# Optimization experiments

Measured on AMD Instinct MI355X. Metric: run time of the kernel, lower is better.

Reference implementation:

```python
import jax, jax.numpy as jnp
import numpy as np

EPS = 1e-5
NUM_GROUPS = 32
NUM_HEADS = 8

def group_norm(x, w, b):
    # x: (B, C, H, W), 32 groups, affine per-channel
    B, C, H, W = x.shape
    xg = x.reshape(B, NUM_GROUPS, C // NUM_GROUPS, H, W)
    mu = xg.mean(axis=(2, 3, 4), keepdims=True)
    var = xg.var(axis=(2, 3, 4), keepdims=True)
    xn = ((xg - mu) * jax.lax.rsqrt(var + EPS)).reshape(B, C, H, W)
    return xn * w[None, :, None, None] + b[None, :, None, None]

def conv1x1(x, w, b):
    # 1x1 conv == per-pixel linear; w: (out, in), x: (B, C, H, W)
    return jnp.einsum('oc,bchw->bohw', w, x) + b[None, :, None, None]

def setup_inputs() -> dict:
    key = jax.random.key(0)
    ks = jax.random.split(key, 4)
    B, C, H, W = 2, 512, 64, 64
    s = 1.0 / np.sqrt(C)
    return {
        'x': jax.random.normal(ks[0], (B, C, H, W), jnp.float32),
        'gn_w': jnp.ones((C,), jnp.float32),
        'gn_b': jnp.zeros((C,), jnp.float32),
        'wq': jax.random.normal(ks[1], (C, C), jnp.float32) * s,
        'bq': jnp.zeros((C,), jnp.float32),
        'wkv': jax.random.normal(ks[2], (2 * C, C), jnp.float32) * s,
        'bkv': jnp.zeros((2 * C,), jnp.float32),
        'wo': jax.random.normal(ks[3], (C, C), jnp.float32) * s,
        'bo': jnp.zeros((C,), jnp.float32),
    }

def reference(x, gn_w, gn_b, wq, bq, wkv, bkv, wo, bo):
    B, C, H, W = x.shape
    hd = C // NUM_HEADS  # head_dim
    residual = x
    x_norm = group_norm(x, gn_w, gn_b)
    q = conv1x1(x_norm, wq, bq).reshape(B, NUM_HEADS, hd, H * W)
    kv = conv1x1(x_norm, wkv, bkv)
    k, v = jnp.split(kv, 2, axis=1)
    k = k.reshape(B, NUM_HEADS, hd, H * W)
    v = v.reshape(B, NUM_HEADS, hd, H * W)
    scale = hd ** (-0.5)
    attn = jnp.einsum('bhdi,bhdj->bhij', q, k) * scale
    attn = jax.nn.softmax(attn, axis=-1)
    out = jnp.einsum('bhij,bhdj->bhdi', attn, v).reshape(B, C, H, W)
    out = conv1x1(out, wo, bo)
    return out + residual
```

## Files before the change

kernel.cpp:

```cpp
#include <hip/hip_runtime.h>
#include <cmath>

typedef __bf16 bf16x8 __attribute__((ext_vector_type(8)));
typedef __bf16 bf16x4 __attribute__((ext_vector_type(4)));
typedef float  f32x4  __attribute__((ext_vector_type(4)));

static __device__ __forceinline__ f32x4 mfma16(bf16x8 a, bf16x8 b, f32x4 c) {
    return __builtin_amdgcn_mfma_f32_16x16x32_bf16(a, b, c, 0, 0, 0);
}

static __device__ __forceinline__ float fast_exp2(float x) {
#if __has_builtin(__builtin_amdgcn_exp2f)
    return __builtin_amdgcn_exp2f(x);
#else
    return exp2f(x);
#endif
}

static __device__ __forceinline__ bf16x8 cvt8(float4 a, float4 b) {
    bf16x8 r;
    r[0] = (__bf16)a.x; r[1] = (__bf16)a.y; r[2] = (__bf16)a.z; r[3] = (__bf16)a.w;
    r[4] = (__bf16)b.x; r[5] = (__bf16)b.y; r[6] = (__bf16)b.z; r[7] = (__bf16)b.w;
    return r;
}

#define OFF_STATS 0
#define OFF_XNT   (4096 + 2u*1024*1024)
#define OFF_QKT   (OFF_XNT + 8u*1024*1024)
#define OFF_V     (OFF_QKT + 16u*1024*1024)
#define OFF_OP    (OFF_V + 8u*1024*1024)
#define CHUNK_O   4194304u
#define CHUNK_L   65536u

__global__ __launch_bounds__(256) void gn_stats(const float* __restrict__ x,
                                                float* __restrict__ stats) {
    int blk = blockIdx.x;
    int bg = blk >> 2, chunk = blk & 3;
    const float* base = x + (size_t)bg * 65536 + (size_t)chunk * 16384;
    float s = 0.f, ss = 0.f;
    for (int i = threadIdx.x; i < 4096; i += 256) {
        float4 v = ((const float4*)base)[i];
        s  += v.x + v.y + v.z + v.w;
        ss += v.x*v.x + v.y*v.y + v.z*v.z + v.w*v.w;
    }
    #pragma unroll
    for (int off = 1; off < 64; off <<= 1) {
        s  += __shfl_xor(s,  off);
        ss += __shfl_xor(ss, off);
    }
    __shared__ float red[8];
    int wave = threadIdx.x >> 6;
    if ((threadIdx.x & 63) == 0) { red[wave*2] = s; red[wave*2+1] = ss; }
    __syncthreads();
    if (threadIdx.x == 0) {
        float S  = red[0] + red[2] + red[4] + red[6];
        float SS = red[1] + red[3] + red[5] + red[7];
        atomicAdd(&stats[bg*2],     S);
        atomicAdd(&stats[bg*2 + 1], SS);
    }
}

__global__ __launch_bounds__(256) void gn_apply(const float* __restrict__ x,
                                                const float* __restrict__ stats,
                                                const float* __restrict__ w,
                                                const float* __restrict__ bgn,
                                                __bf16* __restrict__ xnT) {
    int p0 = blockIdx.x * 64, c0 = blockIdx.y * 64, b = blockIdx.z;
    int tid = threadIdx.x, lane = tid & 63, wave = tid >> 6;
    __shared__ float t[64][69];
    #pragma unroll
    for (int i = 0; i < 16; ++i) {
        int cc = i * 4 + wave;
        int c  = c0 + cc;
        int g  = (b << 5) + (c >> 4);
        float mu  = stats[g*2] * (1.f/65536.f);
        float var = stats[g*2+1] * (1.f/65536.f) - mu*mu;
        float rstd = rsqrtf(var + 1e-5f);
        float val = x[((size_t)(b*512 + c) << 12) + p0 + lane];
        t[cc][lane] = (val - mu) * rstd * w[c] + bgn[c];
    }
    __syncthreads();
    #pragma unroll
    for (int i = 0; i < 16; ++i) {
        int pp = i * 4 + wave;
        xnT[((size_t)(b*4096 + p0 + pp) << 9) + c0 + lane] = (__bf16)t[lane][pp];
    }
}

__global__ __launch_bounds__(256) void gemm_qk_kernel(
    const __bf16* __restrict__ A, const float* __restrict__ Wq,
    const float* __restrict__ Wk,
    const float* __restrict__ bq, const float* __restrict__ bk,
    float qscale, __bf16* __restrict__ out) {
    const int bz = blockIdx.z;
    A += (size_t)bz * 2097152;
    const int m0 = blockIdx.x * 128, n0 = blockIdx.y * 128;
    const int tid = threadIdx.x, lane = tid & 63, wave = tid >> 6;
    const int quad = lane >> 4, l16 = lane & 15;
    const int wm = (wave >> 1) * 64, wn = (wave & 1) * 64;
    const int K = 512;

    __shared__ __attribute__((aligned(16))) __bf16 lds_a[128][40];
    __shared__ __attribute__((aligned(16))) __bf16 lds_b[128][40];

    f32x4 acc[4][4];
    #pragma unroll
    for (int mt = 0; mt < 4; ++mt)
        #pragma unroll
        for (int nt = 0; nt < 4; ++nt)
            #pragma unroll
            for (int r = 0; r < 4; ++r) acc[mt][nt][r] = 0.f;

    const int row_s = tid >> 2;
    const int kc    = (tid & 3) << 3;

    const __bf16* Abase = A + (size_t)(m0 + row_s) * K + kc;
    const int br0 = n0 + row_s, br1 = br0 + 64;
    const float* B0 = (br0 < 512) ? (Wq + (size_t)br0 * K + kc) : (Wk + (size_t)(br0 - 512) * K + kc);
    const float* B1 = (br1 < 512) ? (Wq + (size_t)br1 * K + kc) : (Wk + (size_t)(br1 - 512) * K + kc);

    uint4 ra0, ra1;
    float4 f0a, f0b, f1a, f1b;
    ra0 = *(const uint4*)Abase;
    ra1 = *(const uint4*)(Abase + (size_t)64 * K);
    f0a = *(const float4*)B0;      f0b = *(const float4*)(B0 + 4);
    f1a = *(const float4*)B1;      f1b = *(const float4*)(B1 + 4);

    for (int kt = 0; kt < K; kt += 32) {
        *(uint4*)&lds_a[row_s][kc]       = ra0;
        *(uint4*)&lds_a[row_s + 64][kc]  = ra1;
        *(bf16x8*)&lds_b[row_s][kc]      = cvt8(f0a, f0b);
        *(bf16x8*)&lds_b[row_s + 64][kc] = cvt8(f1a, f1b);
        __syncthreads();
        if (kt + 32 < K) {
            ra0 = *(const uint4*)(Abase + kt + 32);
            ra1 = *(const uint4*)(Abase + kt + 32 + (size_t)64 * K);
            f0a = *(const float4*)(B0 + kt + 32); f0b = *(const float4*)(B0 + kt + 36);
            f1a = *(const float4*)(B1 + kt + 32); f1b = *(const float4*)(B1 + kt + 36);
        }
        bf16x8 af[4], bfr[4];
        #pragma unroll
        for (int mt = 0; mt < 4; ++mt)
            af[mt] = *(const bf16x8*)&lds_a[wm + mt*16 + l16][quad*8];
        #pragma unroll
        for (int nt = 0; nt < 4; ++nt)
            bfr[nt] = *(const bf16x8*)&lds_b[wn + nt*16 + l16][quad*8];
        #pragma unroll
        for (int mt = 0; mt < 4; ++mt)
            #pragma unroll
            for (int nt = 0; nt < 4; ++nt)
                acc[mt][nt] = mfma16(af[mt], bfr[nt], acc[mt][nt]);
        __syncthreads();
    }

    #pragma unroll
    for (int mt = 0; mt < 4; ++mt) {
        const int mrow = m0 + wm + mt*16 + quad*4;
        #pragma unroll
        for (int nt = 0; nt < 4; ++nt) {
            const int ncol = n0 + wn + nt*16 + l16;
            #pragma unroll
            for (int r = 0; r < 4; ++r) {
                const int m = mrow + r;
                float bval = (ncol < 512) ? bq[ncol] : bk[ncol - 512];
                float val = acc[mt][nt][r] + bval;
                if (ncol < 512) val *= qscale;
                out[(size_t)bz * 4194304 + (size_t)m * 1024 + ncol] = (__bf16)val;
            }
        }
    }
}

template<int OUT_F32, int HAS_RES>
__global__ __launch_bounds__(256) void gemm64_kernel(
    const float* __restrict__ A, const __bf16* __restrict__ B,
    const float* __restrict__ bias, const float* __restrict__ res,
    void* __restrict__ out,
    int N, int K, long long strideB, long long strideO) {
    const int bz = blockIdx.z;
    B += strideB * bz;
    const int m0 = blockIdx.x * 64, n0 = blockIdx.y * 128;
    const int tid = threadIdx.x, lane = tid & 63, wave = tid >> 6;
    const int quad = lane >> 4, l16 = lane & 15;
    const int wn = wave * 32;

    __shared__ __attribute__((aligned(16))) __bf16 lds_a[64][40];
    __shared__ __attribute__((aligned(16))) __bf16 lds_b[128][40];

    f32x4 acc[4][2];
    #pragma unroll
    for (int mt = 0; mt < 4; ++mt)
        #pragma unroll
        for (int nt = 0; nt < 2; ++nt)
            #pragma unroll
            for (int r = 0; r < 4; ++r) acc[mt][nt][r] = 0.f;

    const int row_s = tid >> 2;
    const int kc    = (tid & 3) << 3;

    const float*  Abase = A + (size_t)(m0 + row_s) * K + kc;
    const __bf16* Bbase = B + (size_t)(n0 + row_s) * K + kc;
    float4 fa, fb;
    uint4 rb0, rb1;
    fa  = *(const float4*)Abase;  fb = *(const float4*)(Abase + 4);
    rb0 = *(const uint4*)Bbase;
    rb1 = *(const uint4*)(Bbase + (size_t)64 * K);

    for (int kt = 0; kt < K; kt += 32) {
        *(bf16x8*)&lds_a[row_s][kc]     = cvt8(fa, fb);
        *(uint4*)&lds_b[row_s][kc]      = rb0;
        *(uint4*)&lds_b[row_s + 64][kc] = rb1;
        __syncthreads();
        if (kt + 32 < K) {
            fa  = *(const float4*)(Abase + kt + 32); fb = *(const float4*)(Abase + kt + 36);
            rb0 = *(const uint4*)(Bbase + kt + 32);
            rb1 = *(const uint4*)(Bbase + kt + 32 + (size_t)64 * K);
        }
        bf16x8 af[4], bfr[2];
        #pragma unroll
        for (int mt = 0; mt < 4; ++mt)
            af[mt] = *(const bf16x8*)&lds_a[mt*16 + l16][quad*8];
        #pragma unroll
        for (int nt = 0; nt < 2; ++nt)
            bfr[nt] = *(const bf16x8*)&lds_b[wn + nt*16 + l16][quad*8];
        #pragma unroll
        for (int mt = 0; mt < 4; ++mt)
            #pragma unroll
            for (int nt = 0; nt < 2; ++nt)
                acc[mt][nt] = mfma16(af[mt], bfr[nt], acc[mt][nt]);
        __syncthreads();
    }

    #pragma unroll
    for (int mt = 0; mt < 4; ++mt) {
        const int mrow = m0 + mt*16 + quad*4;
        #pragma unroll
        for (int nt = 0; nt < 2; ++nt) {
            const int ncol = n0 + wn + nt*16 + l16;
            #pragma unroll
            for (int r = 0; r < 4; ++r) {
                const int m = mrow + r;
                float val = acc[mt][nt][r] + bias[m];
                const size_t idx = (size_t)strideO * bz + (size_t)m * N + ncol;
                if constexpr (HAS_RES) val += res[idx];
                if constexpr (OUT_F32) ((float*)out)[idx] = val;
                else ((__bf16*)out)[idx] = (__bf16)val;
            }
        }
    }
}

template<int NCH>
__global__ __launch_bounds__(256, 3) void attn_kernel(const __bf16* __restrict__ qkT,
                                                      const __bf16* __restrict__ v,
                                                      __bf16* __restrict__ attnT,
                                                      __bf16* __restrict__ Opart,
                                                      float* __restrict__ Lpart) {
    const int b = blockIdx.y >> 3, h = blockIdx.y & 7;
    const int chunk = (NCH > 1) ? blockIdx.z : 0;
    const int NITER = 64 / NCH;
    const int kt0 = chunk * (4096 / NCH);
    const int tid = threadIdx.x;
    const int wave = tid >> 6, lane = tid & 63;
    const int quad = lane >> 4, l16 = lane & 15;
    const int qbase = blockIdx.x * 256 + wave * 64;

    const __bf16* qkTb = qkT + ((size_t)b << 22);
    const __bf16* vb   = v   + ((size_t)b << 21);

    __shared__ __attribute__((aligned(16))) __bf16 lds_k[64][64];
    __shared__ __attribute__((aligned(16))) __bf16 lds_v[80][64];
    __shared__ __attribute__((aligned(16))) __bf16 lds_p[4][64][36];

    bf16x8 aq[4][2];
    #pragma unroll
    for (int mt = 0; mt < 4; ++mt) {
        const __bf16* qrow = qkTb + (size_t)(qbase + mt*16 + l16) * 1024 + h*64 + quad*8;
        aq[mt][0] = *(const bf16x8*)qrow;
        aq[mt][1] = *(const bf16x8*)(qrow + 32);
    }
    f32x4 o[4][5];
    #pragma unroll
    for (int mt = 0; mt < 4; ++mt)
        #pragma unroll
        for (int dt = 0; dt < 5; ++dt)
            #pragma unroll
            for (int r = 0; r < 4; ++r) o[mt][dt][r] = 0.f;
    const f32x4 kZero = {0.f, 0.f, 0.f, 0.f};

    const int srow = tid >> 2;
    const int sc   = tid & 3;
    const int sw0  = ( sc      ^ (srow & 7)) * 8;
    const int sw1  = ((sc + 4) ^ (srow & 7)) * 8;

    const __bf16* kg0 = qkTb + (size_t)srow * 1024 + 512 + h*64 + sc*8;
    const __bf16* vg0 = vb + ((size_t)(h*64 + srow) << 12) + sc*8;

    if (tid < 64) lds_v[64][tid] = (__bf16)1.0f;

    uint4 ck0, ck1, cv0, cv1;
    {
        const __bf16* kg = kg0 + (size_t)kt0 * 1024;
        const __bf16* vg = vg0 + kt0;
        ck0 = *(const uint4*)kg; ck1 = *(const uint4*)(kg + 32);
        cv0 = *(const uint4*)vg; cv1 = *(const uint4*)(vg + 32);
    }

    for (int it = 0; it < NITER; ++it) {
        *(uint4*)&lds_k[srow][sw0] = ck0;
        *(uint4*)&lds_k[srow][sw1] = ck1;
        *(uint4*)&lds_v[srow][sw0] = cv0;
        *(uint4*)&lds_v[srow][sw1] = cv1;
        __syncthreads();
        if (it + 1 < NITER) {
            const int kt = kt0 + (it + 1) * 64;
            const __bf16* kg = kg0 + (size_t)kt * 1024;
            const __bf16* vg = vg0 + kt;
            ck0 = *(const uint4*)kg; ck1 = *(const uint4*)(kg + 32);
            cv0 = *(const uint4*)vg; cv1 = *(const uint4*)(vg + 32);
        }

        #pragma unroll
        for (int kc = 0; kc < 2; ++kc) {
            #pragma unroll
            for (int ntl = 0; ntl < 2; ++ntl) {
                const int nt = kc*2 + ntl;
                const int kr = nt*16 + l16;
                bf16x8 bk0 = *(const bf16x8*)&lds_k[kr][( quad      ^ (l16 & 7)) * 8];
                bf16x8 bk1 = *(const bf16x8*)&lds_k[kr][((4 + quad) ^ (l16 & 7)) * 8];
                #pragma unroll
                for (int mt = 0; mt < 4; ++mt) {
                    f32x4 s = mfma16(bk1, aq[mt][1], mfma16(bk0, aq[mt][0], kZero));
                    f32x4 p;
                    #pragma unroll
                    for (int r = 0; r < 4; ++r) p[r] = fast_exp2(s[r]);
                    bf16x4 pb = __builtin_convertvector(p, bf16x4);
                    *(bf16x4*)&lds_p[wave][mt*16 + l16][ntl*16 + quad*4] = pb;
                }
            }
            bf16x8 pa[4];
            #pragma unroll
            for (int mt = 0; mt < 4; ++mt) {
                bf16x4 plo = *(const bf16x4*)&lds_p[wave][mt*16 + l16][quad*8];
                bf16x4 phi = *(const bf16x4*)&lds_p[wave][mt*16 + l16][quad*8 + 4];
                pa[mt] = __builtin_shufflevector(plo, phi, 0, 1, 2, 3, 4, 5, 6, 7);
            }
            #pragma unroll
            for (int dt = 0; dt < 5; ++dt) {
                bf16x8 bv = *(const bf16x8*)&lds_v[dt*16 + l16][((kc*4 + quad) ^ (l16 & 7)) * 8];
                #pragma unroll
                for (int mt = 0; mt < 4; ++mt)
                    o[mt][dt] = mfma16(pa[mt], bv, o[mt][dt]);
            }
        }
        __syncthreads();
    }

    if constexpr (NCH > 1) {
        __bf16* Ob = Opart + (size_t)chunk * CHUNK_O;
        #pragma unroll
        for (int mt = 0; mt < 4; ++mt)
            #pragma unroll
            for (int dt = 0; dt < 4; ++dt)
                #pragma unroll
                for (int r = 0; r < 4; ++r) {
                    size_t row = (size_t)b * 4096 + qbase + mt*16 + quad*4 + r;
                    Ob[(row << 9) + (h << 6) + dt*16 + l16] = (__bf16)o[mt][dt][r];
                }
        if (l16 == 0) {
            #pragma unroll
            for (int mt = 0; mt < 4; ++mt)
                #pragma unroll
                for (int r = 0; r < 4; ++r) {
                    int p = qbase + mt*16 + quad*4 + r;
                    Lpart[(size_t)chunk * CHUNK_L + (size_t)((b*8 + h) << 12) + p] = o[mt][4][r];
                }
        }
    } else {
        #pragma unroll
        for (int mt = 0; mt < 4; ++mt) {
            float inv[4];
            #pragma unroll
            for (int r = 0; r < 4; ++r)
                inv[r] = 1.f / __shfl(o[mt][4][r], lane & 48);
            #pragma unroll
            for (int dt = 0; dt < 4; ++dt)
                #pragma unroll
                for (int r = 0; r < 4; ++r) {
                    size_t row = (size_t)b * 4096 + qbase + mt*16 + quad*4 + r;
                    attnT[(row << 9) + (h << 6) + dt*16 + l16] = (__bf16)(o[mt][dt][r] * inv[r]);
                }
        }
    }
}

template<int NCH>
__global__ __launch_bounds__(256) void attn_combine(const __bf16* __restrict__ Opart,
                                                    const float* __restrict__ Lpart,
                                                    __bf16* __restrict__ attnT) {
    int i = blockIdx.x * 256 + threadIdx.x;
    int c4 = i & 127;
    int p  = (i >> 7) & 4095;
    int b  = i >> 19;
    int h  = c4 >> 4;
    size_t lidx = (size_t)((b*8 + h) << 12) + p;
    float l = 0.f;
    #pragma unroll
    for (int ch = 0; ch < NCH; ++ch) l += Lpart[(size_t)ch * CHUNK_L + lidx];
    float inv = 1.f / l;
    size_t oi = ((size_t)(b*4096 + p) << 9) + c4*4;
    float acc[4] = {0.f, 0.f, 0.f, 0.f};
    #pragma unroll
    for (int ch = 0; ch < NCH; ++ch) {
        bf16x4 ov = *(const bf16x4*)&Opart[(size_t)ch * CHUNK_O + oi];
        #pragma unroll
        for (int r = 0; r < 4; ++r) acc[r] += (float)ov[r];
    }
    bf16x4 rv;
    #pragma unroll
    for (int r = 0; r < 4; ++r) rv[r] = (__bf16)(acc[r] * inv);
    *(bf16x4*)&attnT[oi] = rv;
}

extern "C" void kernel_launch(void* const* d_in, const int* in_sizes, int n_in,
                              void* d_out, int out_size, void* d_ws, size_t ws_size,
                              hipStream_t stream) {
    const float* x   = (const float*)d_in[0];
    const float* gnw = (const float*)d_in[1];
    const float* gnb = (const float*)d_in[2];
    const float* wq  = (const float*)d_in[3];
    const float* bq  = (const float*)d_in[4];
    const float* wkv = (const float*)d_in[5];
    const float* bkv = (const float*)d_in[6];
    const float* wo  = (const float*)d_in[7];
    const float* bo  = (const float*)d_in[8];
    float* out = (float*)d_out;

    char* ws = (char*)d_ws;
    float*  stats  = (float*)(ws + OFF_STATS);
    __bf16* xnT    = (__bf16*)(ws + OFF_XNT);
    __bf16* qkT    = (__bf16*)(ws + OFF_QKT);
    __bf16* vv     = (__bf16*)(ws + OFF_V);
    __bf16* Opart  = (__bf16*)(ws + OFF_OP);
    __bf16* attnT  = xnT;

    const size_t need4 = (size_t)OFF_OP + 4u * (CHUNK_O * 2 + CHUNK_L * 4);
    const size_t need2 = (size_t)OFF_OP + 2u * (CHUNK_O * 2 + CHUNK_L * 4);
    const int nch = (ws_size >= need4) ? 4 : (ws_size >= need2 ? 2 : 1);
    float* Lpart = (float*)(ws + OFF_OP + (size_t)nch * CHUNK_O * 2);

    hipMemsetAsync(stats, 0, 512, stream);
    gn_stats<<<256, 256, 0, stream>>>(x, stats);
    gn_apply<<<dim3(64, 8, 2), 256, 0, stream>>>(x, stats, gnw, gnb, xnT);

    const long long S = 2097152LL;
    gemm_qk_kernel<<<dim3(32, 8, 2), 256, 0, stream>>>(
        xnT, wq, wkv, bq, bkv, 0.125f * 1.44269504f, qkT);
    gemm64_kernel<0,0><<<dim3(8, 32, 2), 256, 0, stream>>>(
        wkv + 262144, xnT, bkv + 512, nullptr, vv, 4096, 512, S, S);

    if (nch == 4) {
        attn_kernel<4><<<dim3(16, 16, 4), 256, 0, stream>>>(qkT, vv, nullptr, Opart, Lpart);
        attn_combine<4><<<4096, 256, 0, stream>>>(Opart, Lpart, attnT);
    } else if (nch == 2) {
        attn_kernel<2><<<dim3(16, 16, 2), 256, 0, stream>>>(qkT, vv, nullptr, Opart, Lpart);
        attn_combine<2><<<4096, 256, 0, stream>>>(Opart, Lpart, attnT);
    } else {
        attn_kernel<1><<<dim3(16, 16, 1), 256, 0, stream>>>(qkT, vv, attnT, nullptr, nullptr);
    }

    gemm64_kernel<1,1><<<dim3(8, 32, 2), 256, 0, stream>>>(
        wo, attnT, bo, x, out, 4096, 512, S, S);
}
```

Baseline: 231.7 us.

## Double-buffer attention K/V tiles via direct global-to-LDS loads, use 3 key chunks

Result: slower. 248.7 us (+7.3%).

```diff
diff --git a/kernel.cpp b/kernel.cpp
--- a/kernel.cpp
+++ b/kernel.cpp
@@ -22,6 +22,12 @@
     r[0] = (__bf16)a.x; r[1] = (__bf16)a.y; r[2] = (__bf16)a.z; r[3] = (__bf16)a.w;
     r[4] = (__bf16)b.x; r[5] = (__bf16)b.y; r[6] = (__bf16)b.z; r[7] = (__bf16)b.w;
     return r;
+}
+
+static __device__ __forceinline__ void load_lds16(const __bf16* g, __bf16* l) {
+    __builtin_amdgcn_global_load_lds(
+        (const __attribute__((address_space(1))) unsigned int*)g,
+        (__attribute__((address_space(3))) unsigned int*)l, 16, 0, 0);
 }
 
 #define OFF_STATS 0
@@ -258,8 +264,9 @@
                                                       float* __restrict__ Lpart) {
     const int b = blockIdx.y >> 3, h = blockIdx.y & 7;
     const int chunk = (NCH > 1) ? blockIdx.z : 0;
-    const int NITER = 64 / NCH;
-    const int kt0 = chunk * (4096 / NCH);
+    const int base = 64 / NCH, rem = 64 % NCH;
+    const int niter = base + (chunk < rem ? 1 : 0);
+    const int it_start = chunk * base + (chunk < rem ? chunk : rem);
     const int tid = threadIdx.x;
     const int wave = tid >> 6, lane = tid & 63;
     const int quad = lane >> 4, l16 = lane & 15;
@@ -268,9 +275,9 @@
     const __bf16* qkTb = qkT + ((size_t)b << 22);
     const __bf16* vb   = v   + ((size_t)b << 21);
 
-    __shared__ __attribute__((aligned(16))) __bf16 lds_k[64][64];
-    __shared__ __attribute__((aligned(16))) __bf16 lds_v[80][64];
-    __shared__ __attribute__((aligned(16))) __bf16 lds_p[4][64][36];
+    __shared__ __attribute__((aligned(16))) __bf16 lds_k[2][4096];
+    __shared__ __attribute__((aligned(16))) __bf16 lds_v[2][4096];
+    __shared__ __attribute__((aligned(16))) __bf16 lds_p[4][64*36];
 
     bf16x8 aq[4][2];
     #pragma unroll
@@ -279,6 +286,10 @@
         aq[mt][0] = *(const bf16x8*)qrow;
         aq[mt][1] = *(const bf16x8*)(qrow + 32);
     }
+    bf16x8 vones;
+    #pragma unroll
+    for (int j = 0; j < 8; ++j) vones[j] = (__bf16)1.0f;
+
     f32x4 o[4][5];
     #pragma unroll
     for (int mt = 0; mt < 4; ++mt)
@@ -288,36 +299,31 @@
             for (int r = 0; r < 4; ++r) o[mt][dt][r] = 0.f;
     const f32x4 kZero = {0.f, 0.f, 0.f, 0.f};
 
-    const int srow = tid >> 2;
-    const int sc   = tid & 3;
-    const int sw0  = ( sc      ^ (srow & 7)) * 8;
-    const int sw1  = ((sc + 4) ^ (srow & 7)) * 8;
-
-    const __bf16* kg0 = qkTb + (size_t)srow * 1024 + 512 + h*64 + sc*8;
-    const __bf16* vg0 = vb + ((size_t)(h*64 + srow) << 12) + sc*8;
-
-    if (tid < 64) lds_v[64][tid] = (__bf16)1.0f;
-
-    uint4 ck0, ck1, cv0, cv1;
+    const __bf16* kgl = qkTb + (size_t)lane * 1024 + 512 + h*64;
+    const __bf16* vgl = vb + ((size_t)(h*64 + lane) << 12);
+
     {
-        const __bf16* kg = kg0 + (size_t)kt0 * 1024;
-        const __bf16* vg = vg0 + kt0;
-        ck0 = *(const uint4*)kg; ck1 = *(const uint4*)(kg + 32);
-        cv0 = *(const uint4*)vg; cv1 = *(const uint4*)(vg + 32);
-    }
-
-    for (int it = 0; it < NITER; ++it) {
-        *(uint4*)&lds_k[srow][sw0] = ck0;
-        *(uint4*)&lds_k[srow][sw1] = ck1;
-        *(uint4*)&lds_v[srow][sw0] = cv0;
-        *(uint4*)&lds_v[srow][sw1] = cv1;
-        __syncthreads();
-        if (it + 1 < NITER) {
-            const int kt = kt0 + (it + 1) * 64;
-            const __bf16* kg = kg0 + (size_t)kt * 1024;
-            const __bf16* vg = vg0 + kt;
-            ck0 = *(const uint4*)kg; ck1 = *(const uint4*)(kg + 32);
-            cv0 = *(const uint4*)vg; cv1 = *(const uint4*)(vg + 32);
+        const int kt = it_start * 64;
+        #pragma unroll
+        for (int j = 0; j < 4; ++j) {
+            const int idx = wave*4 + j;
+            if (idx < 8) load_lds16(kgl + (size_t)kt*1024 + idx*8, &lds_k[0][idx*512 + lane*8]);
+            else         load_lds16(vgl + kt + (idx-8)*8,          &lds_v[0][(idx-8)*512 + lane*8]);
+        }
+    }
+    __syncthreads();
+
+    for (int it = 0; it < niter; ++it) {
+        const int cur = it & 1;
+        if (it + 1 < niter) {
+            const int kt = (it_start + it + 1) * 64;
+            const int nxt = cur ^ 1;
+            #pragma unroll
+            for (int j = 0; j < 4; ++j) {
+                const int idx = wave*4 + j;
+                if (idx < 8) load_lds16(kgl + (size_t)kt*1024 + idx*8, &lds_k[nxt][idx*512 + lane*8]);
+                else         load_lds16(vgl + kt + (idx-8)*8,          &lds_v[nxt][(idx-8)*512 + lane*8]);
+            }
         }
 
         #pragma unroll
@@ -326,8 +332,8 @@
             for (int ntl = 0; ntl < 2; ++ntl) {
                 const int nt = kc*2 + ntl;
                 const int kr = nt*16 + l16;
-                bf16x8 bk0 = *(const bf16x8*)&lds_k[kr][( quad      ^ (l16 & 7)) * 8];
-                bf16x8 bk1 = *(const bf16x8*)&lds_k[kr][((4 + quad) ^ (l16 & 7)) * 8];
+                bf16x8 bk0 = *(const bf16x8*)&lds_k[cur][ quad     *512 + kr*8];
+                bf16x8 bk1 = *(const bf16x8*)&lds_k[cur][(4 + quad)*512 + kr*8];
                 #pragma unroll
                 for (int mt = 0; mt < 4; ++mt) {
                     f32x4 s = mfma16(bk1, aq[mt][1], mfma16(bk0, aq[mt][0], kZero));
@@ -335,19 +341,21 @@
                     #pragma unroll
                     for (int r = 0; r < 4; ++r) p[r] = fast_exp2(s[r]);
                     bf16x4 pb = __builtin_convertvector(p, bf16x4);
-                    *(bf16x4*)&lds_p[wave][mt*16 + l16][ntl*16 + quad*4] = pb;
+                    *(bf16x4*)&lds_p[wave][(mt*16 + l16)*36 + ntl*16 + quad*4] = pb;
                 }
             }
             bf16x8 pa[4];
             #pragma unroll
             for (int mt = 0; mt < 4; ++mt) {
-                bf16x4 plo = *(const bf16x4*)&lds_p[wave][mt*16 + l16][quad*8];
-                bf16x4 phi = *(const bf16x4*)&lds_p[wave][mt*16 + l16][quad*8 + 4];
+                bf16x4 plo = *(const bf16x4*)&lds_p[wave][(mt*16 + l16)*36 + quad*8];
+                bf16x4 phi = *(const bf16x4*)&lds_p[wave][(mt*16 + l16)*36 + quad*8 + 4];
                 pa[mt] = __builtin_shufflevector(plo, phi, 0, 1, 2, 3, 4, 5, 6, 7);
             }
             #pragma unroll
             for (int dt = 0; dt < 5; ++dt) {
-                bf16x8 bv = *(const bf16x8*)&lds_v[dt*16 + l16][((kc*4 + quad) ^ (l16 & 7)) * 8];
+                bf16x8 bv = (dt < 4)
+                    ? *(const bf16x8*)&lds_v[cur][(kc*4 + quad)*512 + (dt*16 + l16)*8]
+                    : vones;
                 #pragma unroll
                 for (int mt = 0; mt < 4; ++mt)
                     o[mt][dt] = mfma16(pa[mt], bv, o[mt][dt]);
@@ -379,16 +387,13 @@
     } else {
         #pragma unroll
         for (int mt = 0; mt < 4; ++mt) {
-            float inv[4];
-            #pragma unroll
-            for (int r = 0; r < 4; ++r)
-                inv[r] = 1.f / __shfl(o[mt][4][r], lane & 48);
             #pragma unroll
             for (int dt = 0; dt < 4; ++dt)
                 #pragma unroll
                 for (int r = 0; r < 4; ++r) {
                     size_t row = (size_t)b * 4096 + qbase + mt*16 + quad*4 + r;
-                    attnT[(row << 9) + (h << 6) + dt*16 + l16] = (__bf16)(o[mt][dt][r] * inv[r]);
+                    attnT[(row << 9) + (h << 6) + dt*16 + l16] =
+                        (__bf16)(o[mt][dt][r] / o[mt][4][r]);
                 }
         }
     }
@@ -444,9 +449,9 @@
     __bf16* Opart  = (__bf16*)(ws + OFF_OP);
     __bf16* attnT  = xnT;
 
-    const size_t need4 = (size_t)OFF_OP + 4u * (CHUNK_O * 2 + CHUNK_L * 4);
-    const size_t need2 = (size_t)OFF_OP + 2u * (CHUNK_O * 2 + CHUNK_L * 4);
-    const int nch = (ws_size >= need4) ? 4 : (ws_size >= need2 ? 2 : 1);
+    const size_t per_chunk = (size_t)CHUNK_O * 2 + (size_t)CHUNK_L * 4;
+    const int nch = (ws_size >= (size_t)OFF_OP + 3*per_chunk) ? 3
+                  : (ws_size >= (size_t)OFF_OP + 2*per_chunk) ? 2 : 1;
     float* Lpart = (float*)(ws + OFF_OP + (size_t)nch * CHUNK_O * 2);
 
     hipMemsetAsync(stats, 0, 512, stream);
@@ -459,9 +464,9 @@
     gemm64_kernel<0,0><<<dim3(8, 32, 2), 256, 0, stream>>>(
         wkv + 262144, xnT, bkv + 512, nullptr, vv, 4096, 512, S, S);
 
-    if (nch == 4) {
-        attn_kernel<4><<<dim3(16, 16, 4), 256, 0, stream>>>(qkT, vv, nullptr, Opart, Lpart);
-        attn_combine<4><<<4096, 256, 0, stream>>>(Opart, Lpart, attnT);
+    if (nch == 3) {
+        attn_kernel<3><<<dim3(16, 16, 3), 256, 0, stream>>>(qkT, vv, nullptr, Opart, Lpart);
+        attn_combine<3><<<4096, 256, 0, stream>>>(Opart, Lpart, attnT);
     } else if (nch == 2) {
         attn_kernel<2><<<dim3(16, 16, 2), 256, 0, stream>>>(qkT, vv, nullptr, Opart, Lpart);
         attn_combine<2><<<4096, 256, 0, stream>>>(Opart, Lpart, attnT);
```

## Fuse split-KV attention combine into output projection GEMM

Applied to the files above, without the earlier changes.

New measurement: 261.0 us. 12.6% more time.

```diff
diff --git a/kernel.cpp b/kernel.cpp
--- a/kernel.cpp
+++ b/kernel.cpp
@@ -379,47 +379,144 @@
     } else {
         #pragma unroll
         for (int mt = 0; mt < 4; ++mt) {
-            float inv[4];
-            #pragma unroll
-            for (int r = 0; r < 4; ++r)
-                inv[r] = 1.f / __shfl(o[mt][4][r], lane & 48);
             #pragma unroll
             for (int dt = 0; dt < 4; ++dt)
                 #pragma unroll
                 for (int r = 0; r < 4; ++r) {
                     size_t row = (size_t)b * 4096 + qbase + mt*16 + quad*4 + r;
-                    attnT[(row << 9) + (h << 6) + dt*16 + l16] = (__bf16)(o[mt][dt][r] * inv[r]);
+                    attnT[(row << 9) + (h << 6) + dt*16 + l16] =
+                        (__bf16)(o[mt][dt][r] / o[mt][4][r]);
                 }
         }
     }
 }
 
 template<int NCH>
-__global__ __launch_bounds__(256) void attn_combine(const __bf16* __restrict__ Opart,
-                                                    const float* __restrict__ Lpart,
-                                                    __bf16* __restrict__ attnT) {
+__global__ __launch_bounds__(256) void linv_kernel(const float* __restrict__ Lpart,
+                                                   float* __restrict__ Linv) {
     int i = blockIdx.x * 256 + threadIdx.x;
-    int c4 = i & 127;
-    int p  = (i >> 7) & 4095;
-    int b  = i >> 19;
-    int h  = c4 >> 4;
-    size_t lidx = (size_t)((b*8 + h) << 12) + p;
+    int b = i >> 15;
+    int p = (i >> 3) & 4095;
+    int h = i & 7;
     float l = 0.f;
     #pragma unroll
-    for (int ch = 0; ch < NCH; ++ch) l += Lpart[(size_t)ch * CHUNK_L + lidx];
-    float inv = 1.f / l;
-    size_t oi = ((size_t)(b*4096 + p) << 9) + c4*4;
-    float acc[4] = {0.f, 0.f, 0.f, 0.f};
+    for (int ch = 0; ch < NCH; ++ch)
+        l += Lpart[(size_t)ch * CHUNK_L + (size_t)((b*8 + h) << 12) + p];
+    Linv[i] = 1.f / l;
+}
+
+template<int NCH>
+__global__ __launch_bounds__(256) void gemm_out_kernel(
+    const float* __restrict__ A, const __bf16* __restrict__ Opart,
+    const float* __restrict__ Linv,
+    const float* __restrict__ bias, const float* __restrict__ res,
+    float* __restrict__ out) {
+    const int bz = blockIdx.z;
+    const int N = 4096, K = 512;
+    const int m0 = blockIdx.x * 64, n0 = blockIdx.y * 128;
+    const int tid = threadIdx.x, lane = tid & 63, wave = tid >> 6;
+    const int quad = lane >> 4, l16 = lane & 15;
+    const int wn = wave * 32;
+
+    __shared__ __attribute__((aligned(16))) __bf16 lds_a[64][40];
+    __shared__ __attribute__((aligned(16))) __bf16 lds_b[128][40];
+
+    f32x4 acc[4][2];
+    #pragma unroll
+    for (int mt = 0; mt < 4; ++mt)
+        #pragma unroll
+        for (int nt = 0; nt < 2; ++nt)
+            #pragma unroll
+            for (int r = 0; r < 4; ++r) acc[mt][nt][r] = 0.f;
+
+    const int row_s = tid >> 2;
+    const int kc    = (tid & 3) << 3;
+
+    const float* Abase = A + (size_t)(m0 + row_s) * K + kc;
+    const int p0 = n0 + row_s, p1 = p0 + 64;
+    const __bf16* B0 = Opart + (size_t)bz * 2097152 + (size_t)p0 * K + kc;
+    const __bf16* B1 = Opart + (size_t)bz * 2097152 + (size_t)p1 * K + kc;
+    float il0[8], il1[8];
+    #pragma unroll
+    for (int h = 0; h < 8; ++h) {
+        il0[h] = Linv[((size_t)(bz*4096 + p0) << 3) + h];
+        il1[h] = Linv[((size_t)(bz*4096 + p1) << 3) + h];
+    }
+
+    float4 fa, fb;
+    uint4 rb0[NCH], rb1[NCH];
+    fa = *(const float4*)Abase;  fb = *(const float4*)(Abase + 4);
     #pragma unroll
     for (int ch = 0; ch < NCH; ++ch) {
-        bf16x4 ov = *(const bf16x4*)&Opart[(size_t)ch * CHUNK_O + oi];
-        #pragma unroll
-        for (int r = 0; r < 4; ++r) acc[r] += (float)ov[r];
-    }
-    bf16x4 rv;
-    #pragma unroll
-    for (int r = 0; r < 4; ++r) rv[r] = (__bf16)(acc[r] * inv);
-    *(bf16x4*)&attnT[oi] = rv;
+        rb0[ch] = *(const uint4*)(B0 + (size_t)ch * CHUNK_O);
+        rb1[ch] = *(const uint4*)(B1 + (size_t)ch * CHUNK_O);
+    }
+
+    #pragma unroll
+    for (int hh = 0; hh < 8; ++hh) {
+        #pragma unroll
+        for (int k2 = 0; k2 < 2; ++k2) {
+            const int kt = hh*64 + k2*32;
+            {
+                float s0[8], s1[8];
+                #pragma unroll
+                for (int j = 0; j < 8; ++j) { s0[j] = 0.f; s1[j] = 0.f; }
+                #pragma unroll
+                for (int ch = 0; ch < NCH; ++ch) {
+                    bf16x8 c0 = __builtin_bit_cast(bf16x8, rb0[ch]);
+                    bf16x8 c1 = __builtin_bit_cast(bf16x8, rb1[ch]);
+                    #pragma unroll
+                    for (int j = 0; j < 8; ++j) { s0[j] += (float)c0[j]; s1[j] += (float)c1[j]; }
+                }
+                bf16x8 w0, w1;
+                #pragma unroll
+                for (int j = 0; j < 8; ++j) {
+                    w0[j] = (__bf16)(s0[j] * il0[hh]);
+                    w1[j] = (__bf16)(s1[j] * il1[hh]);
+                }
+                *(bf16x8*)&lds_a[row_s][kc]     = cvt8(fa, fb);
+                *(bf16x8*)&lds_b[row_s][kc]      = w0;
+                *(bf16x8*)&lds_b[row_s + 64][kc] = w1;
+            }
+            __syncthreads();
+            if (kt + 32 < K) {
+                fa = *(const float4*)(Abase + kt + 32); fb = *(const float4*)(Abase + kt + 36);
+                #pragma unroll
+                for (int ch = 0; ch < NCH; ++ch) {
+                    rb0[ch] = *(const uint4*)(B0 + (size_t)ch * CHUNK_O + kt + 32);
+                    rb1[ch] = *(const uint4*)(B1 + (size_t)ch * CHUNK_O + kt + 32);
+                }
+            }
+            bf16x8 af[4], bfr[2];
+            #pragma unroll
+            for (int mt = 0; mt < 4; ++mt)
+                af[mt] = *(const bf16x8*)&lds_a[mt*16 + l16][quad*8];
+            #pragma unroll
+            for (int nt = 0; nt < 2; ++nt)
+                bfr[nt] = *(const bf16x8*)&lds_b[wn + nt*16 + l16][quad*8];
+            #pragma unroll
+            for (int mt = 0; mt < 4; ++mt)
+                #pragma unroll
+                for (int nt = 0; nt < 2; ++nt)
+                    acc[mt][nt] = mfma16(af[mt], bfr[nt], acc[mt][nt]);
+            __syncthreads();
+        }
+    }
+
+    #pragma unroll
+    for (int mt = 0; mt < 4; ++mt) {
+        const int mrow = m0 + mt*16 + quad*4;
+        #pragma unroll
+        for (int nt = 0; nt < 2; ++nt) {
+            const int ncol = n0 + wn + nt*16 + l16;
+            #pragma unroll
+            for (int r = 0; r < 4; ++r) {
+                const int m = mrow + r;
+                const size_t idx = (size_t)bz * 2097152 + (size_t)m * N + ncol;
+                out[idx] = acc[mt][nt][r] + bias[m] + res[idx];
+            }
+        }
+    }
 }
 
 extern "C" void kernel_launch(void* const* d_in, const int* in_sizes, int n_in,
@@ -444,10 +541,12 @@
     __bf16* Opart  = (__bf16*)(ws + OFF_OP);
     __bf16* attnT  = xnT;
 
-    const size_t need4 = (size_t)OFF_OP + 4u * (CHUNK_O * 2 + CHUNK_L * 4);
-    const size_t need2 = (size_t)OFF_OP + 2u * (CHUNK_O * 2 + CHUNK_L * 4);
-    const int nch = (ws_size >= need4) ? 4 : (ws_size >= need2 ? 2 : 1);
+    const size_t per_chunk = (size_t)CHUNK_O * 2 + (size_t)CHUNK_L * 4;
+    const size_t linv_sz = 65536u * 4;
+    const int nch = (ws_size >= (size_t)OFF_OP + 4*per_chunk + linv_sz) ? 4
+                  : (ws_size >= (size_t)OFF_OP + 2*per_chunk + linv_sz) ? 2 : 1;
     float* Lpart = (float*)(ws + OFF_OP + (size_t)nch * CHUNK_O * 2);
+    float* Linv  = Lpart + (size_t)nch * CHUNK_L;
 
     hipMemsetAsync(stats, 0, 512, stream);
     gn_stats<<<256, 256, 0, stream>>>(x, stats);
@@ -461,14 +560,17 @@
 
     if (nch == 4) {
         attn_kernel<4><<<dim3(16, 16, 4), 256, 0, stream>>>(qkT, vv, nullptr, Opart, Lpart);
-        attn_combine<4><<<4096, 256, 0, stream>>>(Opart, Lpart, attnT);
+        linv_kernel<4><<<256, 256, 0, stream>>>(Lpart, Linv);
+        gemm_out_kernel<4><<<dim3(8, 32, 2), 256, 0, stream>>>(
+            wo, Opart, Linv, bo, x, out);
     } else if (nch == 2) {
         attn_kernel<2><<<dim3(16, 16, 2), 256, 0, stream>>>(qkT, vv, nullptr, Opart, Lpart);
-        attn_combine<2><<<4096, 256, 0, stream>>>(Opart, Lpart, attnT);
+        linv_kernel<2><<<256, 256, 0, stream>>>(Lpart, Linv);
+        gemm_out_kernel<2><<<dim3(8, 32, 2), 256, 0, stream>>>(
+            wo, Opart, Linv, bo, x, out);
     } else {
         attn_kernel<1><<<dim3(16, 16, 1), 256, 0, stream>>>(qkT, vv, attnT, nullptr, nullptr);
-    }
-
-    gemm64_kernel<1,1><<<dim3(8, 32, 2), 256, 0, stream>>>(
-        wo, attnT, bo, x, out, 4096, 512, S, S);
-}
+        gemm64_kernel<1,1><<<dim3(8, 32, 2), 256, 0, stream>>>(
+            wo, attnT, bo, x, out, 4096, 512, S, S);
+    }
+}
```
